# Optimization experiments

Hardware: AMD Instinct MI355X
Metric: run time of the kernel (lower is better)

The kernel has to match this reference:

```python
import jax, jax.numpy as jnp
import numpy as np

N, E = 40000, 640000
DIN, C, EDIM = 128, 128, 32  # heads=1, out_channels=128

def setup_inputs() -> dict:
    key = jax.random.key(0)
    ks = jax.random.split(key, 9)
    x = jax.random.normal(ks[0], (N, DIN), dtype=jnp.float32)
    edge_index = jax.random.randint(ks[1], (2, E), 0, N, dtype=jnp.int64)
    edge_attr = jax.random.normal(ks[2], (E, EDIM), dtype=jnp.float32)
    s = 1.0 / np.sqrt(DIN)
    W = jax.random.normal(ks[3], (DIN, C), dtype=jnp.float32) * s
    W_edge = jax.random.normal(ks[4], (EDIM, C), dtype=jnp.float32) / np.sqrt(EDIM)
    att_src = jax.random.normal(ks[5], (C,), dtype=jnp.float32) * s
    att_dst = jax.random.normal(ks[6], (C,), dtype=jnp.float32) * s
    att_edge = jax.random.normal(ks[7], (C,), dtype=jnp.float32) * s
    bias = jnp.zeros((C,), dtype=jnp.float32)
    return {"x": x, "edge_index": edge_index, "edge_attr": edge_attr,
            "W": W, "W_edge": W_edge, "att_src": att_src, "att_dst": att_dst,
            "att_edge": att_edge, "bias": bias}

def reference(x, edge_index, edge_attr, W, W_edge, att_src, att_dst, att_edge, bias):
    # GATConv (heads=1) with edge features
    h = x @ W                      # [N, C] transformed node features
    a_src = h @ att_src            # [N] per-node source attention logits
    a_dst = h @ att_dst            # [N]
    src, dst = edge_index[0], edge_index[1]
    e = edge_attr @ W_edge         # [E, C]
    a_edge = e @ att_edge          # [E]
    alpha = a_src[src] + a_dst[dst] + a_edge            # [E]
    alpha = jax.nn.leaky_relu(alpha, negative_slope=0.2)
    # segment softmax over incoming edges of each destination node
    amax = jax.ops.segment_max(alpha, dst, num_segments=N)
    amax = jnp.where(jnp.isfinite(amax), amax, 0.0)     # empty segments -> -inf guard
    ex = jnp.exp(alpha - amax[dst])
    denom = jax.ops.segment_sum(ex, dst, num_segments=N)
    w = ex / (denom[dst] + 1e-16)                       # PyG softmax epsilon
    out = jax.ops.segment_sum(h[src] * w[:, None], dst, num_segments=N)  # [N, C]
    return out + bias
```

## Files before the change

kernel.cpp:

```cpp
#include <hip/hip_runtime.h>
#include <hip/hip_bf16.h>
#include <hip/hip_fp16.h>


#define DIN 128
#define CCH 128
#define EDIM 32
#define XS_LD 68

__device__ __forceinline__ unsigned pack_bf2(float a, float b) {
    __hip_bfloat16 x = __float2bfloat16(a);
    __hip_bfloat16 y = __float2bfloat16(b);
    unsigned short ux = *(unsigned short*)&x;
    unsigned short uy = *(unsigned short*)&y;
    return (unsigned)ux | ((unsigned)uy << 16);
}

__global__ __launch_bounds__(256) void gemm_h(
    const float* __restrict__ x, const float* __restrict__ W,
    const float* __restrict__ att_src, const float* __restrict__ att_dst,
    unsigned* __restrict__ hb, float* __restrict__ a_src,
    float* __restrict__ a_dst, int N) {
    __shared__ float xs[64 * XS_LD];
    __shared__ float wl[64 * CCH];
    const int t = threadIdx.x;
    const int tx = t & 15;
    const int ty = t >> 4;
    const int row0 = blockIdx.x * 64;

    float acc[4][8];
#pragma unroll
    for (int r = 0; r < 4; ++r)
#pragma unroll
        for (int c = 0; c < 8; ++c) acc[r][c] = 0.0f;

    for (int kh = 0; kh < 2; ++kh) {
        __syncthreads();
        {
            const float4* xg = (const float4*)x;
#pragma unroll
            for (int i = 0; i < 4; ++i) {
                int j4 = t + 256 * i;
                int r = j4 >> 4;
                int k = (j4 & 15) * 4;
                float4 v = xg[(size_t)(row0 + r) * 32 + kh * 16 + (j4 & 15)];
                *(float4*)&xs[r * XS_LD + k] = v;
            }
        }
        {
            const float4* wg = (const float4*)W;
#pragma unroll
            for (int i = 0; i < 8; ++i) {
                int j4 = t + 256 * i;
                int k = j4 >> 5;
                int c4 = j4 & 31;
                float4 v = wg[(size_t)(kh * 64 + k) * 32 + c4];
                *(float4*)&wl[k * CCH + c4 * 4] = v;
            }
        }
        __syncthreads();

#pragma unroll 4
        for (int k4 = 0; k4 < 64; k4 += 4) {
            float xr[4][4];
#pragma unroll
            for (int r = 0; r < 4; ++r) {
                float4 v = *(const float4*)&xs[(ty * 4 + r) * XS_LD + k4];
                xr[r][0] = v.x; xr[r][1] = v.y; xr[r][2] = v.z; xr[r][3] = v.w;
            }
            float wr[4][8];
#pragma unroll
            for (int i = 0; i < 4; ++i) {
                float4 w0 = *(const float4*)&wl[(k4 + i) * CCH + tx * 8];
                float4 w1 = *(const float4*)&wl[(k4 + i) * CCH + tx * 8 + 4];
                wr[i][0] = w0.x; wr[i][1] = w0.y; wr[i][2] = w0.z; wr[i][3] = w0.w;
                wr[i][4] = w1.x; wr[i][5] = w1.y; wr[i][6] = w1.z; wr[i][7] = w1.w;
            }
#pragma unroll
            for (int i = 0; i < 4; ++i)
#pragma unroll
                for (int r = 0; r < 4; ++r)
#pragma unroll
                    for (int c = 0; c < 8; ++c)
                        acc[r][c] += xr[r][i] * wr[i][c];
        }
    }

    float asv[8], adv[8];
#pragma unroll
    for (int c = 0; c < 8; ++c) {
        asv[c] = att_src[tx * 8 + c];
        adv[c] = att_dst[tx * 8 + c];
    }
#pragma unroll
    for (int r = 0; r < 4; ++r) {
        const int row = row0 + ty * 4 + r;
        unsigned u0 = pack_bf2(acc[r][0], acc[r][1]);
        unsigned u1 = pack_bf2(acc[r][2], acc[r][3]);
        unsigned u2 = pack_bf2(acc[r][4], acc[r][5]);
        unsigned u3 = pack_bf2(acc[r][6], acc[r][7]);
        *(uint4*)&hb[(size_t)row * 64 + tx * 4] = make_uint4(u0, u1, u2, u3);
        float ps = 0.0f, pd = 0.0f;
#pragma unroll
        for (int c = 0; c < 8; ++c) {
            ps += acc[r][c] * asv[c];
            pd += acc[r][c] * adv[c];
        }
        ps += __shfl_down(ps, 8, 16);
        pd += __shfl_down(pd, 8, 16);
        ps += __shfl_down(ps, 4, 16);
        pd += __shfl_down(pd, 4, 16);
        ps += __shfl_down(ps, 2, 16);
        pd += __shfl_down(pd, 2, 16);
        ps += __shfl_down(ps, 1, 16);
        pd += __shfl_down(pd, 1, 16);
        if (tx == 0) {
            a_src[row] = ps;
            a_dst[row] = pd;
        }
    }
}

__global__ void compute_vedge(const float* __restrict__ W_edge,
                              const float* __restrict__ att_edge,
                              float* __restrict__ v) {
    int j = threadIdx.x;
    if (j < EDIM) {
        float s = 0.0f;
        for (int c = 0; c < CCH; ++c) s += W_edge[j * CCH + c] * att_edge[c];
        v[j] = s;
    }
}

__global__ void edge_pre(const int* __restrict__ ei, const float* __restrict__ ea,
                         const float* __restrict__ v,
                         const float* __restrict__ a_src,
                         const float* __restrict__ a_dst,
                         unsigned* __restrict__ srec, int* __restrict__ count,
                         int E) {
    __shared__ float vl[EDIM];
    if (threadIdx.x < EDIM) vl[threadIdx.x] = v[threadIdx.x];
    __syncthreads();
    int e = blockIdx.x * blockDim.x + threadIdx.x;
    if (e >= E) return;
    const float4* ea4 = (const float4*)(ea + (size_t)e * EDIM);
    float s = 0.0f;
#pragma unroll
    for (int j = 0; j < 8; ++j) {
        float4 q = ea4[j];
        s += q.x * vl[4 * j] + q.y * vl[4 * j + 1] + q.z * vl[4 * j + 2] +
             q.w * vl[4 * j + 3];
    }
    int sn = ei[e];
    int dn = ei[E + e];
    float alpha = a_src[sn] + a_dst[dn] + s;
    alpha = alpha > 0.0f ? alpha : 0.2f * alpha;
    float ex = __expf(alpha);
    __half hx = __float2half(ex);
    srec[e] = (unsigned)(unsigned short)sn |
              ((unsigned)__half_as_ushort(hx) << 16);
    atomicAdd(&count[dn], 1);
}

__global__ __launch_bounds__(256) void scan_part(const int* __restrict__ count,
                                                 int* __restrict__ bsum, int N4) {
    int i4 = blockIdx.x * 256 + threadIdx.x;
    int s = 0;
    if (i4 < N4) {
        int4 vv = ((const int4*)count)[i4];
        s = vv.x + vv.y + vv.z + vv.w;
    }
#pragma unroll
    for (int off = 32; off; off >>= 1) s += __shfl_down(s, off);
    __shared__ int wsum[4];
    if ((threadIdx.x & 63) == 0) wsum[threadIdx.x >> 6] = s;
    __syncthreads();
    if (threadIdx.x == 0)
        bsum[blockIdx.x] = wsum[0] + wsum[1] + wsum[2] + wsum[3];
}

__global__ void scan_top(int* __restrict__ bsum, int nb) {
    int l = threadIdx.x;
    int orig = (l < nb) ? bsum[l] : 0;
    int v = orig;
#pragma unroll
    for (int off = 1; off < 64; off <<= 1) {
        int u = __shfl_up(v, off);
        if (l >= off) v += u;
    }
    if (l < nb) bsum[l] = v - orig;
}

__global__ __launch_bounds__(256) void scan_apply(const int* __restrict__ count,
                                                  const int* __restrict__ bsum,
                                                  int* __restrict__ cursor,
                                                  int N4) {
    int i4 = blockIdx.x * 256 + threadIdx.x;
    int4 vv = make_int4(0, 0, 0, 0);
    if (i4 < N4) vv = ((const int4*)count)[i4];
    int s = vv.x + vv.y + vv.z + vv.w;
    int lane = threadIdx.x & 63, w = threadIdx.x >> 6;
    int inc = s;
#pragma unroll
    for (int off = 1; off < 64; off <<= 1) {
        int u = __shfl_up(inc, off);
        if (lane >= off) inc += u;
    }
    __shared__ int wt[4];
    if (lane == 63) wt[w] = inc;
    __syncthreads();
    int woff = 0;
    for (int i = 0; i < w; ++i) woff += wt[i];
    int ex = bsum[blockIdx.x] + woff + inc - s;
    if (i4 < N4) {
        int4 o;
        o.x = ex;
        o.y = ex + vv.x;
        o.z = ex + vv.x + vv.y;
        o.w = ex + vv.x + vv.y + vv.z;
        ((int4*)cursor)[i4] = o;
    }
}

__global__ void fill_k(const int* __restrict__ ei, const unsigned* __restrict__ srec,
                       int* __restrict__ cursor, unsigned* __restrict__ pairs,
                       int E) {
    int e = blockIdx.x * blockDim.x + threadIdx.x;
    if (e >= E) return;
    int dn = ei[E + e];
    int p = atomicAdd(&cursor[dn], 1);
    pairs[p] = srec[e];
}

__global__ __launch_bounds__(256) void gather_k(
    const int* __restrict__ count, const int* __restrict__ cursor,
    const unsigned* __restrict__ pairs, const unsigned* __restrict__ hb,
    const float* __restrict__ bias, float* __restrict__ out, int N) {
    int n = blockIdx.x * 4 + (threadIdx.x >> 6);
    int lane = threadIdx.x & 63;
    if (n >= N) return;
    int cnt = count[n];
    int start = cursor[n] - cnt;
    const unsigned* pp = pairs + start;
    float a0 = 0.0f, a1 = 0.0f, sum = 0.0f;
    int j = 0;
    for (; j + 4 <= cnt; j += 4) {
        unsigned r0 = pp[j], r1 = pp[j + 1], r2 = pp[j + 2], r3 = pp[j + 3];
        unsigned q0 = hb[(size_t)(r0 & 0xffffu) * 64 + lane];
        unsigned q1 = hb[(size_t)(r1 & 0xffffu) * 64 + lane];
        unsigned q2 = hb[(size_t)(r2 & 0xffffu) * 64 + lane];
        unsigned q3 = hb[(size_t)(r3 & 0xffffu) * 64 + lane];
        float e0 = __half2float(__ushort_as_half((unsigned short)(r0 >> 16)));
        float e1 = __half2float(__ushort_as_half((unsigned short)(r1 >> 16)));
        float e2 = __half2float(__ushort_as_half((unsigned short)(r2 >> 16)));
        float e3 = __half2float(__ushort_as_half((unsigned short)(r3 >> 16)));
        a0 += e0 * __uint_as_float(q0 << 16);
        a1 += e0 * __uint_as_float(q0 & 0xffff0000u);
        a0 += e1 * __uint_as_float(q1 << 16);
        a1 += e1 * __uint_as_float(q1 & 0xffff0000u);
        a0 += e2 * __uint_as_float(q2 << 16);
        a1 += e2 * __uint_as_float(q2 & 0xffff0000u);
        a0 += e3 * __uint_as_float(q3 << 16);
        a1 += e3 * __uint_as_float(q3 & 0xffff0000u);
        sum += (e0 + e1) + (e2 + e3);
    }
    for (; j < cnt; ++j) {
        unsigned r = pp[j];
        unsigned q = hb[(size_t)(r & 0xffffu) * 64 + lane];
        float ex = __half2float(__ushort_as_half((unsigned short)(r >> 16)));
        a0 += ex * __uint_as_float(q << 16);
        a1 += ex * __uint_as_float(q & 0xffff0000u);
        sum += ex;
    }
    float inv = 1.0f / (sum + 1e-16f);
    float2 bv = *(const float2*)&bias[2 * lane];
    float2 o;
    o.x = a0 * inv + bv.x;
    o.y = a1 * inv + bv.y;
    *(float2*)&out[(size_t)n * CCH + 2 * lane] = o;
}

extern "C" void kernel_launch(void* const* d_in, const int* in_sizes, int n_in,
                              void* d_out, int out_size, void* d_ws, size_t ws_size,
                              hipStream_t stream) {
    const float* x        = (const float*)d_in[0];
    const int*   ei       = (const int*)d_in[1];
    const float* ea       = (const float*)d_in[2];
    const float* W        = (const float*)d_in[3];
    const float* W_edge   = (const float*)d_in[4];
    const float* att_src  = (const float*)d_in[5];
    const float* att_dst  = (const float*)d_in[6];
    const float* att_edge = (const float*)d_in[7];
    const float* bias     = (const float*)d_in[8];
    float* out = (float*)d_out;

    const int N = in_sizes[0] / DIN;
    const int E = in_sizes[2] / EDIM;
    const int N4 = N / 4;
    const int NB = (N4 + 255) / 256;

    char* ws = (char*)d_ws;
    unsigned* hb     = (unsigned*)ws;
    unsigned* pairs  = (unsigned*)(ws + (size_t)N * 64 * 4);
    unsigned* srec   = pairs + E;
    float*    a_src  = (float*)(srec + E);
    float*    a_dst  = a_src + N;
    float*    vedge  = a_dst + N;
    int*      count  = (int*)(vedge + EDIM);
    int*      cursor = count + N;
    int*      bsum   = cursor + N;

    hipMemsetAsync(count, 0, (size_t)N * sizeof(int), stream);

    gemm_h<<<N / 64, 256, 0, stream>>>(x, W, att_src, att_dst, hb, a_src, a_dst, N);
    compute_vedge<<<1, 64, 0, stream>>>(W_edge, att_edge, vedge);
    edge_pre<<<(E + 255) / 256, 256, 0, stream>>>(ei, ea, vedge, a_src, a_dst,
                                                  srec, count, E);
    scan_part<<<NB, 256, 0, stream>>>(count, bsum, N4);
    scan_top<<<1, 64, 0, stream>>>(bsum, NB);
    scan_apply<<<NB, 256, 0, stream>>>(count, bsum, cursor, N4);
    fill_k<<<(E + 255) / 256, 256, 0, stream>>>(ei, srec, cursor, pairs, E);
    gather_k<<<(N + 3) / 4, 256, 0, stream>>>(count, cursor, pairs, hb, bias, out, N);
}
```

Before: 268.1 us.

## Fuse edge logit computation into fill pass and drop intermediate kernels

```diff
diff --git a/kernel.cpp b/kernel.cpp
--- a/kernel.cpp
+++ b/kernel.cpp
@@ -19,14 +19,22 @@
 __global__ __launch_bounds__(256) void gemm_h(
     const float* __restrict__ x, const float* __restrict__ W,
     const float* __restrict__ att_src, const float* __restrict__ att_dst,
-    unsigned* __restrict__ hb, float* __restrict__ a_src,
-    float* __restrict__ a_dst, int N) {
+    const int* __restrict__ ei, unsigned* __restrict__ hb,
+    float* __restrict__ a_src, float* __restrict__ a_dst,
+    int* __restrict__ count, int N, int E) {
     __shared__ float xs[64 * XS_LD];
     __shared__ float wl[64 * CCH];
     const int t = threadIdx.x;
     const int tx = t & 15;
     const int ty = t >> 4;
     const int row0 = blockIdx.x * 64;
+
+    {
+        const int* eid = ei + E;
+        const int stride = gridDim.x * 256;
+        for (int e = blockIdx.x * 256 + t; e < E; e += stride)
+            atomicAdd(&count[eid[e]], 1);
+    }
 
     float acc[4][8];
 #pragma unroll
@@ -121,47 +129,6 @@
     }
 }
 
-__global__ void compute_vedge(const float* __restrict__ W_edge,
-                              const float* __restrict__ att_edge,
-                              float* __restrict__ v) {
-    int j = threadIdx.x;
-    if (j < EDIM) {
-        float s = 0.0f;
-        for (int c = 0; c < CCH; ++c) s += W_edge[j * CCH + c] * att_edge[c];
-        v[j] = s;
-    }
-}
-
-__global__ void edge_pre(const int* __restrict__ ei, const float* __restrict__ ea,
-                         const float* __restrict__ v,
-                         const float* __restrict__ a_src,
-                         const float* __restrict__ a_dst,
-                         unsigned* __restrict__ srec, int* __restrict__ count,
-                         int E) {
-    __shared__ float vl[EDIM];
-    if (threadIdx.x < EDIM) vl[threadIdx.x] = v[threadIdx.x];
-    __syncthreads();
-    int e = blockIdx.x * blockDim.x + threadIdx.x;
-    if (e >= E) return;
-    const float4* ea4 = (const float4*)(ea + (size_t)e * EDIM);
-    float s = 0.0f;
-#pragma unroll
-    for (int j = 0; j < 8; ++j) {
-        float4 q = ea4[j];
-        s += q.x * vl[4 * j] + q.y * vl[4 * j + 1] + q.z * vl[4 * j + 2] +
-             q.w * vl[4 * j + 3];
-    }
-    int sn = ei[e];
-    int dn = ei[E + e];
-    float alpha = a_src[sn] + a_dst[dn] + s;
-    alpha = alpha > 0.0f ? alpha : 0.2f * alpha;
-    float ex = __expf(alpha);
-    __half hx = __float2half(ex);
-    srec[e] = (unsigned)(unsigned short)sn |
-              ((unsigned)__half_as_ushort(hx) << 16);
-    atomicAdd(&count[dn], 1);
-}
-
 __global__ __launch_bounds__(256) void scan_part(const int* __restrict__ count,
                                                  int* __restrict__ bsum, int N4) {
     int i4 = blockIdx.x * 256 + threadIdx.x;
@@ -179,22 +146,17 @@
         bsum[blockIdx.x] = wsum[0] + wsum[1] + wsum[2] + wsum[3];
 }
 
-__global__ void scan_top(int* __restrict__ bsum, int nb) {
-    int l = threadIdx.x;
-    int orig = (l < nb) ? bsum[l] : 0;
-    int v = orig;
-#pragma unroll
-    for (int off = 1; off < 64; off <<= 1) {
-        int u = __shfl_up(v, off);
-        if (l >= off) v += u;
-    }
-    if (l < nb) bsum[l] = v - orig;
-}
-
 __global__ __launch_bounds__(256) void scan_apply(const int* __restrict__ count,
                                                   const int* __restrict__ bsum,
                                                   int* __restrict__ cursor,
                                                   int N4) {
+    __shared__ int s_boff;
+    __shared__ int wt[4];
+    if (threadIdx.x == 0) {
+        int s = 0;
+        for (int i = 0; i < (int)blockIdx.x; ++i) s += bsum[i];
+        s_boff = s;
+    }
     int i4 = blockIdx.x * 256 + threadIdx.x;
     int4 vv = make_int4(0, 0, 0, 0);
     if (i4 < N4) vv = ((const int4*)count)[i4];
@@ -206,31 +168,76 @@
         int u = __shfl_up(inc, off);
         if (lane >= off) inc += u;
     }
-    __shared__ int wt[4];
     if (lane == 63) wt[w] = inc;
     __syncthreads();
     int woff = 0;
     for (int i = 0; i < w; ++i) woff += wt[i];
-    int ex = bsum[blockIdx.x] + woff + inc - s;
+    int exd = s_boff + woff + inc - s;
     if (i4 < N4) {
         int4 o;
-        o.x = ex;
-        o.y = ex + vv.x;
-        o.z = ex + vv.x + vv.y;
-        o.w = ex + vv.x + vv.y + vv.z;
+        o.x = exd;
+        o.y = exd + vv.x;
+        o.z = exd + vv.x + vv.y;
+        o.w = exd + vv.x + vv.y + vv.z;
         ((int4*)cursor)[i4] = o;
     }
 }
 
-__global__ void fill_k(const int* __restrict__ ei, const unsigned* __restrict__ srec,
-                       int* __restrict__ cursor, unsigned* __restrict__ pairs,
-                       int E) {
-    int e = blockIdx.x * blockDim.x + threadIdx.x;
+__global__ __launch_bounds__(256) void edge_fill(
+    const int* __restrict__ ei, const float* __restrict__ ea,
+    const float* __restrict__ W_edge, const float* __restrict__ att_edge,
+    const float* __restrict__ a_src, const float* __restrict__ a_dst,
+    int* __restrict__ cursor, unsigned* __restrict__ pairs, int E) {
+    __shared__ float vpart[8][EDIM];
+    __shared__ float vl[EDIM];
+    const int t = threadIdx.x;
+    {
+        int j = t & 31, seg = t >> 5;
+        const float* wr = W_edge + j * CCH + seg * 16;
+        const float* ar = att_edge + seg * 16;
+        float p = 0.0f;
+#pragma unroll
+        for (int k = 0; k < 16; ++k) p += wr[k] * ar[k];
+        vpart[seg][j] = p;
+    }
+    __syncthreads();
+    if (t < EDIM) {
+        float s = 0.0f;
+#pragma unroll
+        for (int i = 0; i < 8; ++i) s += vpart[i][t];
+        vl[t] = s;
+    }
+    __syncthreads();
+
+    int e = blockIdx.x * 256 + t;
     if (e >= E) return;
+    const float4* ea4 = (const float4*)(ea + (size_t)e * EDIM);
+    float s = 0.0f;
+#pragma unroll
+    for (int j = 0; j < 8; ++j) {
+        float4 q = ea4[j];
+        s += q.x * vl[4 * j] + q.y * vl[4 * j + 1] + q.z * vl[4 * j + 2] +
+             q.w * vl[4 * j + 3];
+    }
+    int sn = ei[e];
     int dn = ei[E + e];
+    float alpha = a_src[sn] + a_dst[dn] + s;
+    alpha = alpha > 0.0f ? alpha : 0.2f * alpha;
+    float ex = __expf(alpha);
+    unsigned rec = (unsigned)(unsigned short)sn |
+                   ((unsigned)__half_as_ushort(__float2half(ex)) << 16);
     int p = atomicAdd(&cursor[dn], 1);
-    pairs[p] = srec[e];
-}
+    pairs[p] = rec;
+}
+
+#define GATHER_EDGE(rec)                                                      \
+    {                                                                         \
+        unsigned q = hb[(size_t)((rec) & 0xffffu) * 64 + lane];               \
+        float exv = __half2float(__ushort_as_half((unsigned short)((rec) >> 16))); \
+        a0 += exv * __uint_as_float(q << 16);                                 \
+        a1 += exv * __uint_as_float(q & 0xffff0000u);                         \
+        sum += exv;                                                           \
+    }
 
 __global__ __launch_bounds__(256) void gather_k(
     const int* __restrict__ count, const int* __restrict__ cursor,
@@ -241,36 +248,63 @@
     if (n >= N) return;
     int cnt = count[n];
     int start = cursor[n] - cnt;
-    const unsigned* pp = pairs + start;
     float a0 = 0.0f, a1 = 0.0f, sum = 0.0f;
     int j = 0;
-    for (; j + 4 <= cnt; j += 4) {
-        unsigned r0 = pp[j], r1 = pp[j + 1], r2 = pp[j + 2], r3 = pp[j + 3];
-        unsigned q0 = hb[(size_t)(r0 & 0xffffu) * 64 + lane];
-        unsigned q1 = hb[(size_t)(r1 & 0xffffu) * 64 + lane];
-        unsigned q2 = hb[(size_t)(r2 & 0xffffu) * 64 + lane];
-        unsigned q3 = hb[(size_t)(r3 & 0xffffu) * 64 + lane];
-        float e0 = __half2float(__ushort_as_half((unsigned short)(r0 >> 16)));
-        float e1 = __half2float(__ushort_as_half((unsigned short)(r1 >> 16)));
-        float e2 = __half2float(__ushort_as_half((unsigned short)(r2 >> 16)));
-        float e3 = __half2float(__ushort_as_half((unsigned short)(r3 >> 16)));
-        a0 += e0 * __uint_as_float(q0 << 16);
-        a1 += e0 * __uint_as_float(q0 & 0xffff0000u);
-        a0 += e1 * __uint_as_float(q1 << 16);
-        a1 += e1 * __uint_as_float(q1 & 0xffff0000u);
-        a0 += e2 * __uint_as_float(q2 << 16);
-        a1 += e2 * __uint_as_float(q2 & 0xffff0000u);
-        a0 += e3 * __uint_as_float(q3 << 16);
-        a1 += e3 * __uint_as_float(q3 & 0xffff0000u);
-        sum += (e0 + e1) + (e2 + e3);
+    int head = (4 - (start & 3)) & 3;
+    if (head > cnt) head = cnt;
+    for (; j < head; ++j) {
+        unsigned r = pairs[start + j];
+        GATHER_EDGE(r);
+    }
+    int nq = (cnt - j) >> 2;
+    if (nq > 0) {
+        const uint4* pp4 = (const uint4*)(pairs + start + j);
+        uint4 cur = pp4[0];
+        for (int g = 0; g + 1 < nq; ++g) {
+            uint4 nxt = pp4[g + 1];
+            unsigned q0 = hb[(size_t)(cur.x & 0xffffu) * 64 + lane];
+            unsigned q1 = hb[(size_t)(cur.y & 0xffffu) * 64 + lane];
+            unsigned q2 = hb[(size_t)(cur.z & 0xffffu) * 64 + lane];
+            unsigned q3 = hb[(size_t)(cur.w & 0xffffu) * 64 + lane];
+            float e0 = __half2float(__ushort_as_half((unsigned short)(cur.x >> 16)));
+            float e1 = __half2float(__ushort_as_half((unsigned short)(cur.y >> 16)));
+            float e2 = __half2float(__ushort_as_half((unsigned short)(cur.z >> 16)));
+            float e3 = __half2float(__ushort_as_half((unsigned short)(cur.w >> 16)));
+            a0 += e0 * __uint_as_float(q0 << 16);
+            a1 += e0 * __uint_as_float(q0 & 0xffff0000u);
+            a0 += e1 * __uint_as_float(q1 << 16);
+            a1 += e1 * __uint_as_float(q1 & 0xffff0000u);
+            a0 += e2 * __uint_as_float(q2 << 16);
+            a1 += e2 * __uint_as_float(q2 & 0xffff0000u);
+            a0 += e3 * __uint_as_float(q3 << 16);
+            a1 += e3 * __uint_as_float(q3 & 0xffff0000u);
+            sum += (e0 + e1) + (e2 + e3);
+            cur = nxt;
+        }
+        {
+            unsigned q0 = hb[(size_t)(cur.x & 0xffffu) * 64 + lane];
+            unsigned q1 = hb[(size_t)(cur.y & 0xffffu) * 64 + lane];
+            unsigned q2 = hb[(size_t)(cur.z & 0xffffu) * 64 + lane];
+            unsigned q3 = hb[(size_t)(cur.w & 0xffffu) * 64 + lane];
+            float e0 = __half2float(__ushort_as_half((unsigned short)(cur.x >> 16)));
+            float e1 = __half2float(__ushort_as_half((unsigned short)(cur.y >> 16)));
+            float e2 = __half2float(__ushort_as_half((unsigned short)(cur.z >> 16)));
+            float e3 = __half2float(__ushort_as_half((unsigned short)(cur.w >> 16)));
+            a0 += e0 * __uint_as_float(q0 << 16);
+            a1 += e0 * __uint_as_float(q0 & 0xffff0000u);
+            a0 += e1 * __uint_as_float(q1 << 16);
+            a1 += e1 * __uint_as_float(q1 & 0xffff0000u);
+            a0 += e2 * __uint_as_float(q2 << 16);
+            a1 += e2 * __uint_as_float(q2 & 0xffff0000u);
+            a0 += e3 * __uint_as_float(q3 << 16);
+            a1 += e3 * __uint_as_float(q3 & 0xffff0000u);
+            sum += (e0 + e1) + (e2 + e3);
+        }
+        j += nq * 4;
     }
     for (; j < cnt; ++j) {
-        unsigned r = pp[j];
-        unsigned q = hb[(size_t)(r & 0xffffu) * 64 + lane];
-        float ex = __half2float(__ushort_as_half((unsigned short)(r >> 16)));
-        a0 += ex * __uint_as_float(q << 16);
-        a1 += ex * __uint_as_float(q & 0xffff0000u);
-        sum += ex;
+        unsigned r = pairs[start + j];
+        GATHER_EDGE(r);
     }
     float inv = 1.0f / (sum + 1e-16f);
     float2 bv = *(const float2*)&bias[2 * lane];
@@ -302,23 +336,19 @@
     char* ws = (char*)d_ws;
     unsigned* hb     = (unsigned*)ws;
     unsigned* pairs  = (unsigned*)(ws + (size_t)N * 64 * 4);
-    unsigned* srec   = pairs + E;
-    float*    a_src  = (float*)(srec + E);
+    float*    a_src  = (float*)(pairs + E);
     float*    a_dst  = a_src + N;
-    float*    vedge  = a_dst + N;
-    int*      count  = (int*)(vedge + EDIM);
+    int*      count  = (int*)(a_dst + N);
     int*      cursor = count + N;
     int*      bsum   = cursor + N;
 
     hipMemsetAsync(count, 0, (size_t)N * sizeof(int), stream);
 
-    gemm_h<<<N / 64, 256, 0, stream>>>(x, W, att_src, att_dst, hb, a_src, a_dst, N);
-    compute_vedge<<<1, 64, 0, stream>>>(W_edge, att_edge, vedge);
-    edge_pre<<<(E + 255) / 256, 256, 0, stream>>>(ei, ea, vedge, a_src, a_dst,
-                                                  srec, count, E);
+    gemm_h<<<N / 64, 256, 0, stream>>>(x, W, att_src, att_dst, ei, hb,
+                                       a_src, a_dst, count, N, E);
     scan_part<<<NB, 256, 0, stream>>>(count, bsum, N4);
-    scan_top<<<1, 64, 0, stream>>>(bsum, NB);
     scan_apply<<<NB, 256, 0, stream>>>(count, bsum, cursor, N4);
-    fill_k<<<(E + 255) / 256, 256, 0, stream>>>(ei, srec, cursor, pairs, E);
+    edge_fill<<<(E + 255) / 256, 256, 0, stream>>>(ei, ea, W_edge, att_edge,
+                                                   a_src, a_dst, cursor, pairs, E);
     gather_k<<<(N + 3) / 4, 256, 0, stream>>>(count, cursor, pairs, hb, bias, out, N);
 }
```

New measurement: 260.6 us. 2.8% less time.
